# Kernel tuning notes

Hardware: AMD Instinct MI355X
Metric: run time of the kernel (lower is better)

Reference implementation:

```python
import jax, jax.numpy as jnp
import numpy as np

NEG_SLOPE = 0.2
CHUNK = 64  # target-node chunk size to bound the [B,c,N,H,D] intermediate


def layer_norm(x, g, b, eps=1e-5):
    mu = jnp.mean(x, axis=-1, keepdims=True)
    var = jnp.mean((x - mu) ** 2, axis=-1, keepdims=True)
    return (x - mu) / jnp.sqrt(var + eps) * g + b


def gatv2_dense(x, Wl, bl, Wr, br, att, bias):
    """GATv2 (PyG semantics, concat=True) on a fully-connected graph with self-loops.
    x: [B,N,Fin]; att: [H,D]. Returns [B,N,H*D].
    e_ij = att_h . leaky_relu(xl_j + xr_i); softmax over sources j; out_i = sum_j a_ij xl_j.
    """
    B, N, _ = x.shape
    H, D = att.shape
    xl = (x @ Wl + bl).reshape(B, N, H, D)  # source-side (lin_l)
    xr = (x @ Wr + br).reshape(B, N, H, D)  # target-side (lin_r)
    nc = N // CHUNK
    xr_ch = jnp.moveaxis(xr.reshape(B, nc, CHUNK, H, D), 1, 0)  # [nc,B,c,H,D]

    @jax.checkpoint
    def per_chunk(xr_c):  # xr_c: [B,c,H,D]
        z = jax.nn.leaky_relu(xr_c[:, :, None] + xl[:, None], NEG_SLOPE)  # [B,c,N,H,D]
        e = jnp.einsum('bcjhd,hd->bcjh', z, att)
        a = jax.nn.softmax(e, axis=2)  # softmax over sources j
        return jnp.einsum('bcjh,bjhd->bchd', a, xl)

    out = jax.lax.map(per_chunk, xr_ch)  # [nc,B,c,H,D]
    return jnp.moveaxis(out, 0, 1).reshape(B, N, H * D) + bias


def setup_inputs() -> dict:
    key = jax.random.key(0)
    ks = jax.random.split(key, 12)
    B, N, Fin, Hd, H, Do = 4, 2048, 32, 32, 4, 32
    f32 = jnp.float32

    def glorot(k, shape, fan_in):
        return jax.random.normal(k, shape, f32) * (1.0 / np.sqrt(fan_in))

    return {
        'x': jax.random.normal(ks[0], (B, N, Fin), f32),
        'embedding': jax.random.normal(ks[1], (N, Hd), f32),
        # layer 1: in=Fin, heads=H, head dim=Hd
        'Wl1': glorot(ks[2], (Fin, H * Hd), Fin), 'bl1': jnp.zeros((H * Hd,), f32),
        'Wr1': glorot(ks[3], (Fin, H * Hd), Fin), 'br1': jnp.zeros((H * Hd,), f32),
        'att1': glorot(ks[4], (H, Hd), Hd), 'bias1': jnp.zeros((H * Hd,), f32),
        'ln1_g': jnp.ones((H * Hd,), f32), 'ln1_b': jnp.zeros((H * Hd,), f32),
        # layer 2: in=H*Hd, heads=H, head dim=Do
        'Wl2': glorot(ks[5], (H * Hd, H * Do), H * Hd), 'bl2': jnp.zeros((H * Do,), f32),
        'Wr2': glorot(ks[6], (H * Hd, H * Do), H * Hd), 'br2': jnp.zeros((H * Do,), f32),
        'att2': glorot(ks[7], (H, Do), Do), 'bias2': jnp.zeros((H * Do,), f32),
        'ln2_g': jnp.ones((H * Do,), f32), 'ln2_b': jnp.zeros((H * Do,), f32),
    }


def reference(x, embedding, Wl1, bl1, Wr1, br1, att1, bias1, ln1_g, ln1_b,
              Wl2, bl2, Wr2, br2, att2, bias2, ln2_g, ln2_b):
    # AdaptiveAdjacency: cosine-similarity gram matrix. Its values are generically
    # all nonzero, so adj[b].nonzero() yields a fully-connected edge list including
    # self-loops; only the connectivity (dense) is consumed downstream.
    ne = embedding / jnp.linalg.norm(embedding, axis=1, keepdims=True)
    adj = ne @ ne.T  # [N,N]; connectivity only (dense), values unused by GATv2
    del adj

    h = layer_norm(gatv2_dense(x, Wl1, bl1, Wr1, br1, att1, bias1), ln1_g, ln1_b)
    h = jax.nn.relu(h)
    # dropout(p=0.3) is identity in eval mode
    out = layer_norm(gatv2_dense(h, Wl2, bl2, Wr2, br2, att2, bias2), ln2_g, ln2_b)
    return out
```

## Files before the change

### kernel.cpp

```cpp
#include <hip/hip_runtime.h>
#include <math.h>

#define LOG2E 1.4426950408889634f

#if __has_builtin(__builtin_amdgcn_exp2f)
#define EXP2(x) __builtin_amdgcn_exp2f(x)
#else
#define EXP2(x) exp2f(x)
#endif

constexpr int B_ = 4, N_ = 2048, H_ = 4, D_ = 32, HD_ = 128;
constexpr int BH_ = B_ * H_;
constexpr int ROWS_ = BH_ * N_;
constexpr size_t M_ = (size_t)ROWS_ * D_;

typedef float v4f __attribute__((ext_vector_type(4)));
typedef _Float16 h2 __attribute__((ext_vector_type(2)));

static __device__ __forceinline__ h2 habs2(h2 z) {
    unsigned int t = __builtin_bit_cast(unsigned int, z) & 0x7FFF7FFFu;
    return __builtin_bit_cast(h2, t);
}
static __device__ __forceinline__ h2 hadd2u(unsigned int a, unsigned int b) {
    return __builtin_bit_cast(h2, a) + __builtin_bit_cast(h2, b);
}
static __device__ __forceinline__ h2 u2h(unsigned int a) {
    return __builtin_bit_cast(h2, a);
}

__global__ __launch_bounds__(256) void k_linear(
    const float* __restrict__ x,
    const float* __restrict__ Wl, const float* __restrict__ bl,
    const float* __restrict__ Wr, const float* __restrict__ br,
    float* __restrict__ xl, unsigned short* __restrict__ xlh,
    unsigned short* __restrict__ xrh, unsigned int* __restrict__ xlpT, int K)
{
    __shared__ __align__(16) float xs[32 * 128];
    const int tid = threadIdx.x;
    const int r0 = blockIdx.x * 32;
    const float4* src = (const float4*)(x + (size_t)r0 * K);
    float4* dst = (float4*)xs;
    for (int idx = tid; idx < 8 * K; idx += 256) dst[idx] = src[idx];
    __syncthreads();

    const int c  = tid & 127;
    const int rg = tid >> 7;
    float accl[16], accr[16];
    const float blv = bl[c], brv = br[c];
    #pragma unroll
    for (int r = 0; r < 16; r++) { accl[r] = blv; accr[r] = brv; }
    #pragma unroll 8
    for (int k = 0; k < K; k++) {
        const float wl = Wl[k * HD_ + c];
        const float wr = Wr[k * HD_ + c];
        #pragma unroll
        for (int r = 0; r < 16; r++) {
            const float xv = xs[(rg * 16 + r) * K + k];
            accl[r] = fmaf(xv, wl, accl[r]);
            accr[r] = fmaf(xv, wr, accr[r]);
        }
    }
    const int h = c >> 5, d = c & 31;
    #pragma unroll
    for (int r = 0; r < 16; r++) {
        const int row = r0 + rg * 16 + r;
        const int b = row >> 11, n = row & (N_ - 1);
        const size_t o = (((size_t)(b * H_ + h)) * N_ + n) * D_ + d;
        xl[o] = accl[r];
        xlh[o] = __builtin_bit_cast(unsigned short, (_Float16)accl[r]);
        xrh[o] = __builtin_bit_cast(unsigned short, (_Float16)accr[r]);
    }
    #pragma unroll
    for (int r = 0; r < 16; r += 2) {
        const int row = r0 + rg * 16 + r;
        const int b = row >> 11, n = row & (N_ - 1);
        h2 pr;
        pr.x = (_Float16)accl[r];
        pr.y = (_Float16)accl[r + 1];
        const size_t o = (((size_t)(b * H_ + h)) * (N_ / 2) + (n >> 1)) * D_ + d;
        xlpT[o] = __builtin_bit_cast(unsigned int, pr);
    }
}

__global__ __launch_bounds__(256) void k_u(
    const float* __restrict__ xl, const float* __restrict__ att,
    float* __restrict__ u)
{
    const int idx = blockIdx.x * 256 + threadIdx.x;
    const int h = (idx / N_) & (H_ - 1);
    const float4* a4 = (const float4*)(att + h * D_);
    const float4* l4 = (const float4*)(xl + (size_t)idx * D_);
    float su = 0.f;
    #pragma unroll
    for (int q = 0; q < 8; q++) {
        const float4 a = a4[q], lv = l4[q];
        su += a.x * lv.x + a.y * lv.y + a.z * lv.z + a.w * lv.w;
    }
    u[idx] = 0.6f * LOG2E * su;
}

__global__ __launch_bounds__(512) void k_bound(
    const unsigned int* __restrict__ xlh, const unsigned int* __restrict__ xrh,
    const float* __restrict__ u, const float* __restrict__ att,
    float* __restrict__ bound, unsigned int* __restrict__ tch)
{
    __shared__ float redA[16][33];
    __shared__ float redB[16][33];
    __shared__ float clv[32];
    __shared__ float tca[32];
    __shared__ float redu[512];
    const int bh = blockIdx.x, h = bh & (H_ - 1), t = threadIdx.x;

    if (bh < H_ && t < 16) {
        h2 v;
        v.x = (_Float16)(att[bh * D_ + 2 * t]     * (0.4f * LOG2E));
        v.y = (_Float16)(att[bh * D_ + 2 * t + 1] * (0.4f * LOG2E));
        tch[bh * 16 + t] = __builtin_bit_cast(unsigned int, v);
    }
    if (t < 16) {
        _Float16 a = (_Float16)(att[h * D_ + 2 * t]     * (0.4f * LOG2E));
        _Float16 b = (_Float16)(att[h * D_ + 2 * t + 1] * (0.4f * LOG2E));
        tca[2 * t]     = fabsf((float)a);
        tca[2 * t + 1] = fabsf((float)b);
    }
    const unsigned int* xb = xlh + (size_t)bh * N_ * 16;
    const int p = t & 15, rg = t >> 4;
    float m0 = 0.f, m1 = 0.f;
    for (int r = rg; r < N_; r += 32) {
        h2 z = __builtin_bit_cast(h2, xb[r * 16 + p] & 0x7FFF7FFFu);
        m0 = fmaxf(m0, (float)z.x);
        m1 = fmaxf(m1, (float)z.y);
    }
    redA[p][rg] = m0; redB[p][rg] = m1;
    const float* ub = u + (size_t)bh * N_;
    float um = -1e30f;
    for (int r = t; r < N_; r += 512) um = fmaxf(um, ub[r]);
    redu[t] = um;
    __syncthreads();
    if (t < 16) {
        float a = 0.f, b = 0.f;
        for (int g = 0; g < 32; g++) { a = fmaxf(a, redA[t][g]); b = fmaxf(b, redB[t][g]); }
        clv[2 * t] = a; clv[2 * t + 1] = b;
    }
    for (int s = 256; s > 0; s >>= 1) {
        if (t < s) redu[t] = fmaxf(redu[t], redu[t + s]);
        __syncthreads();
    }
    const float umax = redu[0];
    const unsigned int* xrb = xrh + (size_t)bh * N_ * 16;
    for (int r = t; r < N_; r += 512) {
        float s = 0.f;
        #pragma unroll
        for (int k = 0; k < 16; k++) {
            h2 z = __builtin_bit_cast(h2, xrb[r * 16 + k] & 0x7FFF7FFFu);
            s += tca[2 * k] * (clv[2 * k] + (float)z.x)
               + tca[2 * k + 1] * (clv[2 * k + 1] + (float)z.y);
        }
        bound[bh * N_ + r] = umax + s + 0.25f;
    }
}

__global__ __launch_bounds__(256)
__attribute__((amdgpu_waves_per_eu(3, 4)))
void k_attn(
    const unsigned int* __restrict__ xlh,
    const unsigned int* __restrict__ xlpT,
    const unsigned int* __restrict__ xrh,
    const float* __restrict__ u, const float* __restrict__ bound,
    const unsigned int* __restrict__ tch,
    float* __restrict__ P, float* __restrict__ lb, int jlen)
{
    const int tid = threadIdx.x, lane = tid & 63, wid = tid >> 6;
    const int t128 = blockIdx.x & 127, part = blockIdx.x >> 7;
    const int bh = t128 >> 3;
    const int h  = bh & (H_ - 1);
    const int row = bh * N_ + (t128 & 7) * 256 + wid * 64 + lane;

    unsigned int tcs[16];
    #pragma unroll
    for (int k = 0; k < 16; k++)
        tcs[k] = __builtin_amdgcn_readfirstlane(tch[h * 16 + k]);

    unsigned int xrp[16];
    {
        const uint4* s = (const uint4*)(xrh + (size_t)row * 16);
        const uint4 a = s[0], b = s[1], c = s[2], d = s[3];
        xrp[0]=a.x; xrp[1]=a.y; xrp[2]=a.z; xrp[3]=a.w;
        xrp[4]=b.x; xrp[5]=b.y; xrp[6]=b.z; xrp[7]=b.w;
        xrp[8]=c.x; xrp[9]=c.y; xrp[10]=c.z; xrp[11]=c.w;
        xrp[12]=d.x; xrp[13]=d.y; xrp[14]=d.z; xrp[15]=d.w;
    }
    const float negb = -bound[row];

    float l = 0.f;
    float o[32];
    #pragma unroll
    for (int k = 0; k < 32; k++) o[k] = 0.f;

    const unsigned int* xlh_b = xlh + (size_t)bh * N_ * 16;
    const unsigned int* xlt_b = xlpT + (size_t)bh * (N_ / 2) * 32;
    const float* u_b = u + (size_t)bh * N_;

    const int jpb = (part * jlen) >> 1, jpe = jpb + (jlen >> 1);
    for (int jp = jpb; jp < jpe; jp++) {
        const unsigned int* w0 = xlh_b + (size_t)(2 * jp) * 16;
        const unsigned int* w1 = w0 + 16;
        float e0 = u_b[2 * jp]     + negb;
        float f0 = 0.f, e1 = u_b[2 * jp + 1] + negb, f1 = 0.f;
        #pragma unroll
        for (int k = 0; k < 16; k += 2) {
            e0 = __builtin_amdgcn_fdot2(habs2(hadd2u(w0[k],     xrp[k])),     u2h(tcs[k]),     e0, false);
            f0 = __builtin_amdgcn_fdot2(habs2(hadd2u(w0[k + 1], xrp[k + 1])), u2h(tcs[k + 1]), f0, false);
            e1 = __builtin_amdgcn_fdot2(habs2(hadd2u(w1[k],     xrp[k])),     u2h(tcs[k]),     e1, false);
            f1 = __builtin_amdgcn_fdot2(habs2(hadd2u(w1[k + 1], xrp[k + 1])), u2h(tcs[k + 1]), f1, false);
        }
        const float p0 = EXP2(e0 + f0);
        const float p1 = EXP2(e1 + f1);
        const h2 p01 = __builtin_bit_cast(h2, __builtin_amdgcn_cvt_pkrtz(p0, p1));
        h2 ones; ones.x = (_Float16)1.f; ones.y = (_Float16)1.f;
        l = __builtin_amdgcn_fdot2(p01, ones, l, false);
        const unsigned int* vp = xlt_b + (size_t)jp * 32;
        #pragma unroll
        for (int d = 0; d < 32; d++)
            o[d] = __builtin_amdgcn_fdot2(p01, u2h(vp[d]), o[d], false);
    }

    float* Pp = P + (size_t)part * M_ + (size_t)row * D_;
    #pragma unroll
    for (int k = 0; k < 8; k++) {
        v4f w;
        w.x = o[4*k]; w.y = o[4*k+1]; w.z = o[4*k+2]; w.w = o[4*k+3];
        ((v4f*)Pp)[k] = w;
    }
    lb[part * ROWS_ + row] = l;
}

template <int JS>
__global__ __launch_bounds__(64) void k_comb_ln(
    const float* __restrict__ P, const float* __restrict__ lb,
    const float* __restrict__ bias, const float* __restrict__ g,
    const float* __restrict__ bta, float* __restrict__ outp, int do_relu)
{
    const int row = blockIdx.x;
    const int b = row >> 11, n = row & (N_ - 1);
    const int t = threadIdx.x;
    const int c0 = t, c1 = t + 64;
    const int bh0 = b * H_ + (c0 >> 5), bh1 = b * H_ + (c1 >> 5);
    const size_t i0 = ((size_t)bh0 * N_ + n) * D_ + (c0 & 31);
    const size_t i1 = ((size_t)bh1 * N_ + n) * D_ + (c1 & 31);
    float a0 = 0.f, a1 = 0.f, L0 = 0.f, L1 = 0.f;
    #pragma unroll
    for (int s = 0; s < JS; s++) {
        a0 += P[(size_t)s * M_ + i0];
        a1 += P[(size_t)s * M_ + i1];
        L0 += lb[s * ROWS_ + bh0 * N_ + n];
        L1 += lb[s * ROWS_ + bh1 * N_ + n];
    }
    const float x0 = a0 / L0 + bias[c0];
    const float x1 = a1 / L1 + bias[c1];
    float s = x0 + x1;
    #pragma unroll
    for (int w = 1; w < 64; w <<= 1) s += __shfl_xor(s, w);
    const float mu = s * (1.f / 128.f);
    const float d0 = x0 - mu, d1 = x1 - mu;
    float q = d0 * d0 + d1 * d1;
    #pragma unroll
    for (int w = 1; w < 64; w <<= 1) q += __shfl_xor(q, w);
    const float rstd = rsqrtf(q * (1.f / 128.f) + 1e-5f);
    float y0 = d0 * rstd * g[c0] + bta[c0];
    float y1 = d1 * rstd * g[c1] + bta[c1];
    if (do_relu) { y0 = fmaxf(y0, 0.f); y1 = fmaxf(y1, 0.f); }
    outp[(size_t)row * HD_ + c0] = y0;
    outp[(size_t)row * HD_ + c1] = y1;
}

extern "C" void kernel_launch(void* const* d_in, const int* in_sizes, int n_in,
                              void* d_out, int out_size, void* d_ws, size_t ws_size,
                              hipStream_t stream) {
    const float* x    = (const float*)d_in[0];
    const float* Wl1  = (const float*)d_in[2];
    const float* bl1  = (const float*)d_in[3];
    const float* Wr1  = (const float*)d_in[4];
    const float* br1  = (const float*)d_in[5];
    const float* att1 = (const float*)d_in[6];
    const float* bias1= (const float*)d_in[7];
    const float* ln1g = (const float*)d_in[8];
    const float* ln1b = (const float*)d_in[9];
    const float* Wl2  = (const float*)d_in[10];
    const float* bl2  = (const float*)d_in[11];
    const float* Wr2  = (const float*)d_in[12];
    const float* br2  = (const float*)d_in[13];
    const float* att2 = (const float*)d_in[14];
    const float* bias2= (const float*)d_in[15];
    const float* ln2g = (const float*)d_in[16];
    const float* ln2b = (const float*)d_in[17];

    float* ws = (float*)d_ws;
    float* xl = ws;
    unsigned short* xlh = (unsigned short*)(xl + M_);
    unsigned short* xrh = xlh + M_;
    unsigned int* xlpT = (unsigned int*)(xrh + M_);
    float* u     = xl + (size_t)(2.5 * M_);
    float* bound = u + ROWS_;
    unsigned int* tch = (unsigned int*)(bound + ROWS_);

    int js = 1;
    for (int cand = 8; cand >= 1; cand >>= 1) {
        const size_t need = ((size_t)(3.5 * M_) + 2 * ROWS_ + 64
                             + (size_t)cand * (M_ + ROWS_)) * sizeof(float);
        if (ws_size >= need) { js = cand; break; }
    }
    const int jlen = N_ / js;

    float* P  = (float*)(tch + 64);
    float* lb = P + (size_t)js * M_;
    float* h  = lb + (size_t)js * ROWS_;
    float* outf = (float*)d_out;

    const int BN = B_ * N_;
    k_linear<<<BN / 32, 256, 0, stream>>>(x, Wl1, bl1, Wr1, br1, xl, xlh, xrh, xlpT, 32);
    k_u<<<ROWS_ / 256, 256, 0, stream>>>(xl, att1, u);
    k_bound<<<BH_, 512, 0, stream>>>((const unsigned int*)xlh, (const unsigned int*)xrh,
                                     u, att1, bound, tch);
    k_attn<<<128 * js, 256, 0, stream>>>((const unsigned int*)xlh, xlpT,
                                         (const unsigned int*)xrh, u, bound, tch, P, lb, jlen);
    if      (js == 8) k_comb_ln<8><<<BN, 64, 0, stream>>>(P, lb, bias1, ln1g, ln1b, h, 1);
    else if (js == 4) k_comb_ln<4><<<BN, 64, 0, stream>>>(P, lb, bias1, ln1g, ln1b, h, 1);
    else if (js == 2) k_comb_ln<2><<<BN, 64, 0, stream>>>(P, lb, bias1, ln1g, ln1b, h, 1);
    else              k_comb_ln<1><<<BN, 64, 0, stream>>>(P, lb, bias1, ln1g, ln1b, h, 1);
    k_linear<<<BN / 32, 256, 0, stream>>>(h, Wl2, bl2, Wr2, br2, xl, xlh, xrh, xlpT, 128);
    k_u<<<ROWS_ / 256, 256, 0, stream>>>(xl, att2, u);
    k_bound<<<BH_, 512, 0, stream>>>((const unsigned int*)xlh, (const unsigned int*)xrh,
                                     u, att2, bound, tch);
    k_attn<<<128 * js, 256, 0, stream>>>((const unsigned int*)xlh, xlpT,
                                         (const unsigned int*)xrh, u, bound, tch, P, lb, jlen);
    if      (js == 8) k_comb_ln<8><<<BN, 64, 0, stream>>>(P, lb, bias2, ln2g, ln2b, outf, 0);
    else if (js == 4) k_comb_ln<4><<<BN, 64, 0, stream>>>(P, lb, bias2, ln2g, ln2b, outf, 0);
    else if (js == 2) k_comb_ln<2><<<BN, 64, 0, stream>>>(P, lb, bias2, ln2g, ln2b, outf, 0);
    else              k_comb_ln<1><<<BN, 64, 0, stream>>>(P, lb, bias2, ln2g, ln2b, outf, 0);
}
```

Baseline: 489.3 us.

## Software-pipeline attention loop with double-buffered loads and SGPR-operand dot asm

```diff
diff --git a/kernel.cpp b/kernel.cpp
--- a/kernel.cpp
+++ b/kernel.cpp
@@ -17,16 +17,12 @@
 typedef float v4f __attribute__((ext_vector_type(4)));
 typedef _Float16 h2 __attribute__((ext_vector_type(2)));
 
-static __device__ __forceinline__ h2 habs2(h2 z) {
-    unsigned int t = __builtin_bit_cast(unsigned int, z) & 0x7FFF7FFFu;
-    return __builtin_bit_cast(h2, t);
-}
-static __device__ __forceinline__ h2 hadd2u(unsigned int a, unsigned int b) {
-    return __builtin_bit_cast(h2, a) + __builtin_bit_cast(h2, b);
-}
-static __device__ __forceinline__ h2 u2h(unsigned int a) {
-    return __builtin_bit_cast(h2, a);
-}
+static __device__ __forceinline__ unsigned int absadd2(unsigned int a, unsigned int b) {
+    h2 s = __builtin_bit_cast(h2, a) + __builtin_bit_cast(h2, b);
+    return __builtin_bit_cast(unsigned int, s) & 0x7FFF7FFFu;
+}
+#define SDOT(acc, a, sb) asm("v_dot2_f32_f16 %0, %1, %2, %0" : "+v"(acc) : "v"(a), "s"(sb))
+#define VDOT(acc, a, vb) asm("v_dot2_f32_f16 %0, %1, %2, %0" : "+v"(acc) : "v"(a), "v"(vb))
 
 __global__ __launch_bounds__(256) void k_linear(
     const float* __restrict__ x,
@@ -161,7 +157,7 @@
 }
 
 __global__ __launch_bounds__(256)
-__attribute__((amdgpu_waves_per_eu(3, 4)))
+__attribute__((amdgpu_waves_per_eu(2, 4)))
 void k_attn(
     const unsigned int* __restrict__ xlh,
     const unsigned int* __restrict__ xlpT,
@@ -190,7 +186,8 @@
         xrp[8]=c.x; xrp[9]=c.y; xrp[10]=c.z; xrp[11]=c.w;
         xrp[12]=d.x; xrp[13]=d.y; xrp[14]=d.z; xrp[15]=d.w;
     }
-    const float negb = -bound[row];
+    const float negb = 12.0f - bound[row];
+    const unsigned int ONES2 = 0x3C003C00u;
 
     float l = 0.f;
     float o[32];
@@ -202,28 +199,86 @@
     const float* u_b = u + (size_t)bh * N_;
 
     const int jpb = (part * jlen) >> 1, jpe = jpb + (jlen >> 1);
-    for (int jp = jpb; jp < jpe; jp++) {
-        const unsigned int* w0 = xlh_b + (size_t)(2 * jp) * 16;
-        const unsigned int* w1 = w0 + 16;
-        float e0 = u_b[2 * jp]     + negb;
-        float f0 = 0.f, e1 = u_b[2 * jp + 1] + negb, f1 = 0.f;
-        #pragma unroll
-        for (int k = 0; k < 16; k += 2) {
-            e0 = __builtin_amdgcn_fdot2(habs2(hadd2u(w0[k],     xrp[k])),     u2h(tcs[k]),     e0, false);
-            f0 = __builtin_amdgcn_fdot2(habs2(hadd2u(w0[k + 1], xrp[k + 1])), u2h(tcs[k + 1]), f0, false);
-            e1 = __builtin_amdgcn_fdot2(habs2(hadd2u(w1[k],     xrp[k])),     u2h(tcs[k]),     e1, false);
-            f1 = __builtin_amdgcn_fdot2(habs2(hadd2u(w1[k + 1], xrp[k + 1])), u2h(tcs[k + 1]), f1, false);
-        }
-        const float p0 = EXP2(e0 + f0);
-        const float p1 = EXP2(e1 + f1);
-        const h2 p01 = __builtin_bit_cast(h2, __builtin_amdgcn_cvt_pkrtz(p0, p1));
-        h2 ones; ones.x = (_Float16)1.f; ones.y = (_Float16)1.f;
-        l = __builtin_amdgcn_fdot2(p01, ones, l, false);
-        const unsigned int* vp = xlt_b + (size_t)jp * 32;
-        #pragma unroll
-        for (int d = 0; d < 32; d++)
-            o[d] = __builtin_amdgcn_fdot2(p01, u2h(vp[d]), o[d], false);
-    }
+
+#define LOADS(S0, S1, S2, S3, S4, S5, S6, S7, UU0, UU1, JP)                    \
+    {                                                                           \
+        const uint4* _w = (const uint4*)(xlh_b + (size_t)(2 * (JP)) * 16);     \
+        S0 = _w[0]; S1 = _w[1]; S2 = _w[2]; S3 = _w[3];                        \
+        S4 = _w[4]; S5 = _w[5]; S6 = _w[6]; S7 = _w[7];                        \
+        UU0 = u_b[2 * (JP)]; UU1 = u_b[2 * (JP) + 1];                          \
+    }
+#define COMPUTE(S0, S1, S2, S3, S4, S5, S6, S7, UU0, UU1, JP)                  \
+    {                                                                           \
+        const uint4* _vp = (const uint4*)(xlt_b + (size_t)(JP) * 32);          \
+        uint4 _v0 = _vp[0], _v1 = _vp[1], _v2 = _vp[2], _v3 = _vp[3];          \
+        float _e0 = UU0 + negb, _f0 = 0.f, _e1 = UU1 + negb, _f1 = 0.f;        \
+        SDOT(_e0, absadd2(S0.x, xrp[0]),  tcs[0]);                             \
+        SDOT(_f0, absadd2(S0.y, xrp[1]),  tcs[1]);                             \
+        SDOT(_e0, absadd2(S0.z, xrp[2]),  tcs[2]);                             \
+        SDOT(_f0, absadd2(S0.w, xrp[3]),  tcs[3]);                             \
+        SDOT(_e0, absadd2(S1.x, xrp[4]),  tcs[4]);                             \
+        SDOT(_f0, absadd2(S1.y, xrp[5]),  tcs[5]);                             \
+        SDOT(_e0, absadd2(S1.z, xrp[6]),  tcs[6]);                             \
+        SDOT(_f0, absadd2(S1.w, xrp[7]),  tcs[7]);                             \
+        SDOT(_e0, absadd2(S2.x, xrp[8]),  tcs[8]);                             \
+        SDOT(_f0, absadd2(S2.y, xrp[9]),  tcs[9]);                             \
+        SDOT(_e0, absadd2(S2.z, xrp[10]), tcs[10]);                            \
+        SDOT(_f0, absadd2(S2.w, xrp[11]), tcs[11]);                            \
+        SDOT(_e0, absadd2(S3.x, xrp[12]), tcs[12]);                            \
+        SDOT(_f0, absadd2(S3.y, xrp[13]), tcs[13]);                            \
+        SDOT(_e0, absadd2(S3.z, xrp[14]), tcs[14]);                            \
+        SDOT(_f0, absadd2(S3.w, xrp[15]), tcs[15]);                            \
+        SDOT(_e1, absadd2(S4.x, xrp[0]),  tcs[0]);                             \
+        SDOT(_f1, absadd2(S4.y, xrp[1]),  tcs[1]);                             \
+        SDOT(_e1, absadd2(S4.z, xrp[2]),  tcs[2]);                             \
+        SDOT(_f1, absadd2(S4.w, xrp[3]),  tcs[3]);                             \
+        SDOT(_e1, absadd2(S5.x, xrp[4]),  tcs[4]);                             \
+        SDOT(_f1, absadd2(S5.y, xrp[5]),  tcs[5]);                             \
+        SDOT(_e1, absadd2(S5.z, xrp[6]),  tcs[6]);                             \
+        SDOT(_f1, absadd2(S5.w, xrp[7]),  tcs[7]);                             \
+        SDOT(_e1, absadd2(S6.x, xrp[8]),  tcs[8]);                             \
+        SDOT(_f1, absadd2(S6.y, xrp[9]),  tcs[9]);                             \
+        SDOT(_e1, absadd2(S6.z, xrp[10]), tcs[10]);                            \
+        SDOT(_f1, absadd2(S6.w, xrp[11]), tcs[11]);                            \
+        SDOT(_e1, absadd2(S7.x, xrp[12]), tcs[12]);                            \
+        SDOT(_f1, absadd2(S7.y, xrp[13]), tcs[13]);                            \
+        SDOT(_e1, absadd2(S7.z, xrp[14]), tcs[14]);                            \
+        SDOT(_f1, absadd2(S7.w, xrp[15]), tcs[15]);                            \
+        const float _p0 = EXP2(_e0 + _f0);                                     \
+        const float _p1 = EXP2(_e1 + _f1);                                     \
+        const unsigned int _p01 = __builtin_bit_cast(unsigned int,             \
+            __builtin_amdgcn_cvt_pkrtz(_p0, _p1));                             \
+        VDOT(l, _p01, ONES2);                                                  \
+        VDOT(o[0],  _p01, _v0.x); VDOT(o[1],  _p01, _v0.y);                    \
+        VDOT(o[2],  _p01, _v0.z); VDOT(o[3],  _p01, _v0.w);                    \
+        VDOT(o[4],  _p01, _v1.x); VDOT(o[5],  _p01, _v1.y);                    \
+        VDOT(o[6],  _p01, _v1.z); VDOT(o[7],  _p01, _v1.w);                    \
+        VDOT(o[8],  _p01, _v2.x); VDOT(o[9],  _p01, _v2.y);                    \
+        VDOT(o[10], _p01, _v2.z); VDOT(o[11], _p01, _v2.w);                    \
+        VDOT(o[12], _p01, _v3.x); VDOT(o[13], _p01, _v3.y);                    \
+        VDOT(o[14], _p01, _v3.z); VDOT(o[15], _p01, _v3.w);                    \
+        uint4 _v4 = _vp[4], _v5 = _vp[5], _v6 = _vp[6], _v7 = _vp[7];          \
+        VDOT(o[16], _p01, _v4.x); VDOT(o[17], _p01, _v4.y);                    \
+        VDOT(o[18], _p01, _v4.z); VDOT(o[19], _p01, _v4.w);                    \
+        VDOT(o[20], _p01, _v5.x); VDOT(o[21], _p01, _v5.y);                    \
+        VDOT(o[22], _p01, _v5.z); VDOT(o[23], _p01, _v5.w);                    \
+        VDOT(o[24], _p01, _v6.x); VDOT(o[25], _p01, _v6.y);                    \
+        VDOT(o[26], _p01, _v6.z); VDOT(o[27], _p01, _v6.w);                    \
+        VDOT(o[28], _p01, _v7.x); VDOT(o[29], _p01, _v7.y);                    \
+        VDOT(o[30], _p01, _v7.z); VDOT(o[31], _p01, _v7.w);                    \
+    }
+
+    uint4 A0, A1, A2, A3, A4, A5, A6, A7; float AU0, AU1;
+    uint4 B0, B1, B2, B3, B4, B5, B6, B7; float BU0, BU1;
+    LOADS(A0, A1, A2, A3, A4, A5, A6, A7, AU0, AU1, jpb);
+    for (int jp = jpb; jp < jpe; jp += 2) {
+        LOADS(B0, B1, B2, B3, B4, B5, B6, B7, BU0, BU1, jp + 1);
+        COMPUTE(A0, A1, A2, A3, A4, A5, A6, A7, AU0, AU1, jp);
+        LOADS(A0, A1, A2, A3, A4, A5, A6, A7, AU0, AU1, jp + 2);
+        COMPUTE(B0, B1, B2, B3, B4, B5, B6, B7, BU0, BU1, jp + 1);
+    }
+#undef LOADS
+#undef COMPUTE
 
     float* Pp = P + (size_t)part * M_ + (size_t)row * D_;
     #pragma unroll
```

Result: no change. 492.0 us (+0.6%).

## Stage source tiles in LDS and use inline-asm dot2 with SGPR operands in attention

Applied to the files above, without the earlier changes.

```diff
diff --git a/kernel.cpp b/kernel.cpp
--- a/kernel.cpp
+++ b/kernel.cpp
@@ -17,16 +17,12 @@
 typedef float v4f __attribute__((ext_vector_type(4)));
 typedef _Float16 h2 __attribute__((ext_vector_type(2)));
 
-static __device__ __forceinline__ h2 habs2(h2 z) {
-    unsigned int t = __builtin_bit_cast(unsigned int, z) & 0x7FFF7FFFu;
-    return __builtin_bit_cast(h2, t);
-}
-static __device__ __forceinline__ h2 hadd2u(unsigned int a, unsigned int b) {
-    return __builtin_bit_cast(h2, a) + __builtin_bit_cast(h2, b);
-}
-static __device__ __forceinline__ h2 u2h(unsigned int a) {
-    return __builtin_bit_cast(h2, a);
-}
+static __device__ __forceinline__ unsigned int absadd2(unsigned int a, unsigned int b) {
+    h2 s = __builtin_bit_cast(h2, a) + __builtin_bit_cast(h2, b);
+    return __builtin_bit_cast(unsigned int, s) & 0x7FFF7FFFu;
+}
+#define SDOT(acc, a, sb) asm("v_dot2_f32_f16 %0, %1, %2, %0" : "+v"(acc) : "v"(a), "s"(sb))
+#define VDOT(acc, a, vb) asm("v_dot2_f32_f16 %0, %1, %2, %0" : "+v"(acc) : "v"(a), "v"(vb))
 
 __global__ __launch_bounds__(256) void k_linear(
     const float* __restrict__ x,
@@ -160,9 +156,7 @@
     }
 }
 
-__global__ __launch_bounds__(256)
-__attribute__((amdgpu_waves_per_eu(3, 4)))
-void k_attn(
+__global__ __launch_bounds__(256) void k_attn(
     const unsigned int* __restrict__ xlh,
     const unsigned int* __restrict__ xlpT,
     const unsigned int* __restrict__ xrh,
@@ -170,11 +164,14 @@
     const unsigned int* __restrict__ tch,
     float* __restrict__ P, float* __restrict__ lb, int jlen)
 {
-    const int tid = threadIdx.x, lane = tid & 63, wid = tid >> 6;
+    __shared__ __align__(16) uint4 s_xlh[1024];
+    __shared__ __align__(16) uint4 s_xlt[1024];
+    __shared__ float s_u[256];
+    const int tid = threadIdx.x;
     const int t128 = blockIdx.x & 127, part = blockIdx.x >> 7;
     const int bh = t128 >> 3;
     const int h  = bh & (H_ - 1);
-    const int row = bh * N_ + (t128 & 7) * 256 + wid * 64 + lane;
+    const int row = bh * N_ + (t128 & 7) * 256 + tid;
 
     unsigned int tcs[16];
     #pragma unroll
@@ -190,39 +187,96 @@
         xrp[8]=c.x; xrp[9]=c.y; xrp[10]=c.z; xrp[11]=c.w;
         xrp[12]=d.x; xrp[13]=d.y; xrp[14]=d.z; xrp[15]=d.w;
     }
-    const float negb = -bound[row];
+    const float negb = 12.0f - bound[row];
+    const unsigned int ONES2 = 0x3C003C00u;
 
     float l = 0.f;
     float o[32];
     #pragma unroll
     for (int k = 0; k < 32; k++) o[k] = 0.f;
 
-    const unsigned int* xlh_b = xlh + (size_t)bh * N_ * 16;
-    const unsigned int* xlt_b = xlpT + (size_t)bh * (N_ / 2) * 32;
+    const uint4* gx = (const uint4*)(xlh + (size_t)bh * N_ * 16);
+    const uint4* gv = (const uint4*)(xlpT + (size_t)bh * (N_ / 2) * 32);
     const float* u_b = u + (size_t)bh * N_;
 
-    const int jpb = (part * jlen) >> 1, jpe = jpb + (jlen >> 1);
-    for (int jp = jpb; jp < jpe; jp++) {
-        const unsigned int* w0 = xlh_b + (size_t)(2 * jp) * 16;
-        const unsigned int* w1 = w0 + 16;
-        float e0 = u_b[2 * jp]     + negb;
-        float f0 = 0.f, e1 = u_b[2 * jp + 1] + negb, f1 = 0.f;
+    const int jbeg = part * jlen;
+    for (int jt = 0; jt < jlen; jt += 256) {
+        if (jt) __syncthreads();
+        const int j0 = jbeg + jt;
         #pragma unroll
-        for (int k = 0; k < 16; k += 2) {
-            e0 = __builtin_amdgcn_fdot2(habs2(hadd2u(w0[k],     xrp[k])),     u2h(tcs[k]),     e0, false);
-            f0 = __builtin_amdgcn_fdot2(habs2(hadd2u(w0[k + 1], xrp[k + 1])), u2h(tcs[k + 1]), f0, false);
-            e1 = __builtin_amdgcn_fdot2(habs2(hadd2u(w1[k],     xrp[k])),     u2h(tcs[k]),     e1, false);
-            f1 = __builtin_amdgcn_fdot2(habs2(hadd2u(w1[k + 1], xrp[k + 1])), u2h(tcs[k + 1]), f1, false);
+        for (int k = 0; k < 4; k++)
+            s_xlh[tid + 256 * k] = gx[(size_t)j0 * 4 + tid + 256 * k];
+        #pragma unroll
+        for (int k = 0; k < 4; k++)
+            s_xlt[tid + 256 * k] = gv[(size_t)(j0 >> 1) * 8 + tid + 256 * k];
+        s_u[tid] = u_b[j0 + tid];
+        __syncthreads();
+
+        for (int ljp = 0; ljp < 128; ljp++) {
+            const uint4 S0 = s_xlh[8 * ljp + 0], S1 = s_xlh[8 * ljp + 1];
+            const uint4 S2 = s_xlh[8 * ljp + 2], S3 = s_xlh[8 * ljp + 3];
+            const uint4 S4 = s_xlh[8 * ljp + 4], S5 = s_xlh[8 * ljp + 5];
+            const uint4 S6 = s_xlh[8 * ljp + 6], S7 = s_xlh[8 * ljp + 7];
+            float e0 = s_u[2 * ljp] + negb, f0 = 0.f;
+            float e1 = s_u[2 * ljp + 1] + negb, f1 = 0.f;
+            SDOT(e0, absadd2(S0.x, xrp[0]),  tcs[0]);
+            SDOT(f0, absadd2(S0.y, xrp[1]),  tcs[1]);
+            SDOT(e0, absadd2(S0.z, xrp[2]),  tcs[2]);
+            SDOT(f0, absadd2(S0.w, xrp[3]),  tcs[3]);
+            SDOT(e0, absadd2(S1.x, xrp[4]),  tcs[4]);
+            SDOT(f0, absadd2(S1.y, xrp[5]),  tcs[5]);
+            SDOT(e0, absadd2(S1.z, xrp[6]),  tcs[6]);
+            SDOT(f0, absadd2(S1.w, xrp[7]),  tcs[7]);
+            SDOT(e0, absadd2(S2.x, xrp[8]),  tcs[8]);
+            SDOT(f0, absadd2(S2.y, xrp[9]),  tcs[9]);
+            SDOT(e0, absadd2(S2.z, xrp[10]), tcs[10]);
+            SDOT(f0, absadd2(S2.w, xrp[11]), tcs[11]);
+            SDOT(e0, absadd2(S3.x, xrp[12]), tcs[12]);
+            SDOT(f0, absadd2(S3.y, xrp[13]), tcs[13]);
+            SDOT(e0, absadd2(S3.z, xrp[14]), tcs[14]);
+            SDOT(f0, absadd2(S3.w, xrp[15]), tcs[15]);
+            SDOT(e1, absadd2(S4.x, xrp[0]),  tcs[0]);
+            SDOT(f1, absadd2(S4.y, xrp[1]),  tcs[1]);
+            SDOT(e1, absadd2(S4.z, xrp[2]),  tcs[2]);
+            SDOT(f1, absadd2(S4.w, xrp[3]),  tcs[3]);
+            SDOT(e1, absadd2(S5.x, xrp[4]),  tcs[4]);
+            SDOT(f1, absadd2(S5.y, xrp[5]),  tcs[5]);
+            SDOT(e1, absadd2(S5.z, xrp[6]),  tcs[6]);
+            SDOT(f1, absadd2(S5.w, xrp[7]),  tcs[7]);
+            SDOT(e1, absadd2(S6.x, xrp[8]),  tcs[8]);
+            SDOT(f1, absadd2(S6.y, xrp[9]),  tcs[9]);
+            SDOT(e1, absadd2(S6.z, xrp[10]), tcs[10]);
+            SDOT(f1, absadd2(S6.w, xrp[11]), tcs[11]);
+            SDOT(e1, absadd2(S7.x, xrp[12]), tcs[12]);
+            SDOT(f1, absadd2(S7.y, xrp[13]), tcs[13]);
+            SDOT(e1, absadd2(S7.z, xrp[14]), tcs[14]);
+            SDOT(f1, absadd2(S7.w, xrp[15]), tcs[15]);
+            const float p0 = EXP2(e0 + f0);
+            const float p1 = EXP2(e1 + f1);
+            const unsigned int p01 = __builtin_bit_cast(unsigned int,
+                __builtin_amdgcn_cvt_pkrtz(p0, p1));
+            VDOT(l, p01, ONES2);
+            const uint4 V0 = s_xlt[8 * ljp + 0], V1 = s_xlt[8 * ljp + 1];
+            const uint4 V2 = s_xlt[8 * ljp + 2], V3 = s_xlt[8 * ljp + 3];
+            VDOT(o[0],  p01, V0.x); VDOT(o[1],  p01, V0.y);
+            VDOT(o[2],  p01, V0.z); VDOT(o[3],  p01, V0.w);
+            VDOT(o[4],  p01, V1.x); VDOT(o[5],  p01, V1.y);
+            VDOT(o[6],  p01, V1.z); VDOT(o[7],  p01, V1.w);
+            VDOT(o[8],  p01, V2.x); VDOT(o[9],  p01, V2.y);
+            VDOT(o[10], p01, V2.z); VDOT(o[11], p01, V2.w);
+            VDOT(o[12], p01, V3.x); VDOT(o[13], p01, V3.y);
+            VDOT(o[14], p01, V3.z); VDOT(o[15], p01, V3.w);
+            const uint4 V4 = s_xlt[8 * ljp + 4], V5 = s_xlt[8 * ljp + 5];
+            const uint4 V6 = s_xlt[8 * ljp + 6], V7 = s_xlt[8 * ljp + 7];
+            VDOT(o[16], p01, V4.x); VDOT(o[17], p01, V4.y);
+            VDOT(o[18], p01, V4.z); VDOT(o[19], p01, V4.w);
+            VDOT(o[20], p01, V5.x); VDOT(o[21], p01, V5.y);
+            VDOT(o[22], p01, V5.z); VDOT(o[23], p01, V5.w);
+            VDOT(o[24], p01, V6.x); VDOT(o[25], p01, V6.y);
+            VDOT(o[26], p01, V6.z); VDOT(o[27], p01, V6.w);
+            VDOT(o[28], p01, V7.x); VDOT(o[29], p01, V7.y);
+            VDOT(o[30], p01, V7.z); VDOT(o[31], p01, V7.w);
         }
-        const float p0 = EXP2(e0 + f0);
-        const float p1 = EXP2(e1 + f1);
-        const h2 p01 = __builtin_bit_cast(h2, __builtin_amdgcn_cvt_pkrtz(p0, p1));
-        h2 ones; ones.x = (_Float16)1.f; ones.y = (_Float16)1.f;
-        l = __builtin_amdgcn_fdot2(p01, ones, l, false);
-        const unsigned int* vp = xlt_b + (size_t)jp * 32;
-        #pragma unroll
-        for (int d = 0; d < 32; d++)
-            o[d] = __builtin_amdgcn_fdot2(p01, u2h(vp[d]), o[d], false);
     }
 
     float* Pp = P + (size_t)part * M_ + (size_t)row * D_;
```

Measured after the change: 429.7 us. 12.2% less time.

## Stage source rows in LDS and use inline-asm fma_mix for attention

Applied to the files above, without the earlier changes.

```diff
diff --git a/kernel.cpp b/kernel.cpp
--- a/kernel.cpp
+++ b/kernel.cpp
@@ -17,23 +17,12 @@
 typedef float v4f __attribute__((ext_vector_type(4)));
 typedef _Float16 h2 __attribute__((ext_vector_type(2)));
 
-static __device__ __forceinline__ h2 habs2(h2 z) {
-    unsigned int t = __builtin_bit_cast(unsigned int, z) & 0x7FFF7FFFu;
-    return __builtin_bit_cast(h2, t);
-}
-static __device__ __forceinline__ h2 hadd2u(unsigned int a, unsigned int b) {
-    return __builtin_bit_cast(h2, a) + __builtin_bit_cast(h2, b);
-}
-static __device__ __forceinline__ h2 u2h(unsigned int a) {
-    return __builtin_bit_cast(h2, a);
-}
-
 __global__ __launch_bounds__(256) void k_linear(
     const float* __restrict__ x,
     const float* __restrict__ Wl, const float* __restrict__ bl,
     const float* __restrict__ Wr, const float* __restrict__ br,
     float* __restrict__ xl, unsigned short* __restrict__ xlh,
-    unsigned short* __restrict__ xrh, unsigned int* __restrict__ xlpT, int K)
+    unsigned short* __restrict__ xrh, int K)
 {
     __shared__ __align__(16) float xs[32 * 128];
     const int tid = threadIdx.x;
@@ -70,16 +59,6 @@
         xlh[o] = __builtin_bit_cast(unsigned short, (_Float16)accl[r]);
         xrh[o] = __builtin_bit_cast(unsigned short, (_Float16)accr[r]);
     }
-    #pragma unroll
-    for (int r = 0; r < 16; r += 2) {
-        const int row = r0 + rg * 16 + r;
-        const int b = row >> 11, n = row & (N_ - 1);
-        h2 pr;
-        pr.x = (_Float16)accl[r];
-        pr.y = (_Float16)accl[r + 1];
-        const size_t o = (((size_t)(b * H_ + h)) * (N_ / 2) + (n >> 1)) * D_ + d;
-        xlpT[o] = __builtin_bit_cast(unsigned int, pr);
-    }
 }
 
 __global__ __launch_bounds__(256) void k_u(
@@ -160,26 +139,41 @@
     }
 }
 
-__global__ __launch_bounds__(256)
-__attribute__((amdgpu_waves_per_eu(3, 4)))
-void k_attn(
+
+#define SG(K, EA, EB)                                                          \
+    "v_pk_add_f16 %[z], %[s" K "], %[x" K "]\n\t"                              \
+    "v_and_b32 %[z], %[mk], %[z]\n\t"                                          \
+    "v_fma_mix_f32 %[" EA "], %[tl" K "], %[z], %[" EA "] op_sel:[0,0,0] op_sel_hi:[0,1,0]\n\t" \
+    "v_fma_mix_f32 %[" EB "], %[th" K "], %[z], %[" EB "] op_sel:[0,1,0] op_sel_hi:[0,1,0]\n\t"
+
+#define PVG(KL, KH, SK)                                                        \
+    "v_fma_mix_f32 %[o" KL "], %[p], %[s" SK "], %[o" KL "] op_sel:[0,0,0] op_sel_hi:[0,1,0]\n\t" \
+    "v_fma_mix_f32 %[o" KH "], %[p], %[s" SK "], %[o" KH "] op_sel:[0,1,0] op_sel_hi:[0,1,0]\n\t"
+
+__global__ __launch_bounds__(256) void k_attn(
     const unsigned int* __restrict__ xlh,
-    const unsigned int* __restrict__ xlpT,
     const unsigned int* __restrict__ xrh,
     const float* __restrict__ u, const float* __restrict__ bound,
     const unsigned int* __restrict__ tch,
     float* __restrict__ P, float* __restrict__ lb, int jlen)
 {
-    const int tid = threadIdx.x, lane = tid & 63, wid = tid >> 6;
+    __shared__ __align__(16) uint4 s_xlh[1024];
+    __shared__ float s_u[256];
+    __shared__ float s_pad[4096];
+    const int tid = threadIdx.x;
     const int t128 = blockIdx.x & 127, part = blockIdx.x >> 7;
     const int bh = t128 >> 3;
     const int h  = bh & (H_ - 1);
-    const int row = bh * N_ + (t128 & 7) * 256 + wid * 64 + lane;
-
-    unsigned int tcs[16];
-    #pragma unroll
-    for (int k = 0; k < 16; k++)
-        tcs[k] = __builtin_amdgcn_readfirstlane(tch[h * 16 + k]);
+    const int row = bh * N_ + (t128 & 7) * 256 + tid;
+    if (jlen < 0) s_pad[tid] = 0.f;
+
+    float tf[32];
+    #pragma unroll
+    for (int k = 0; k < 16; k++) {
+        const h2 t2 = __builtin_bit_cast(h2, tch[h * 16 + k]);
+        tf[2 * k]     = (float)t2.x;
+        tf[2 * k + 1] = (float)t2.y;
+    }
 
     unsigned int xrp[16];
     {
@@ -191,38 +185,82 @@
         xrp[12]=d.x; xrp[13]=d.y; xrp[14]=d.z; xrp[15]=d.w;
     }
     const float negb = -bound[row];
+    const unsigned int kAbsMask = 0x7FFF7FFFu;
 
     float l = 0.f;
     float o[32];
     #pragma unroll
     for (int k = 0; k < 32; k++) o[k] = 0.f;
 
-    const unsigned int* xlh_b = xlh + (size_t)bh * N_ * 16;
-    const unsigned int* xlt_b = xlpT + (size_t)bh * (N_ / 2) * 32;
+    const uint4* gx = (const uint4*)(xlh + (size_t)bh * N_ * 16);
     const float* u_b = u + (size_t)bh * N_;
 
-    const int jpb = (part * jlen) >> 1, jpe = jpb + (jlen >> 1);
-    for (int jp = jpb; jp < jpe; jp++) {
-        const unsigned int* w0 = xlh_b + (size_t)(2 * jp) * 16;
-        const unsigned int* w1 = w0 + 16;
-        float e0 = u_b[2 * jp]     + negb;
-        float f0 = 0.f, e1 = u_b[2 * jp + 1] + negb, f1 = 0.f;
+    const int jbeg = part * jlen;
+    for (int jt = 0; jt < jlen; jt += 256) {
+        if (jt) __syncthreads();
+        const int j0 = jbeg + jt;
         #pragma unroll
-        for (int k = 0; k < 16; k += 2) {
-            e0 = __builtin_amdgcn_fdot2(habs2(hadd2u(w0[k],     xrp[k])),     u2h(tcs[k]),     e0, false);
-            f0 = __builtin_amdgcn_fdot2(habs2(hadd2u(w0[k + 1], xrp[k + 1])), u2h(tcs[k + 1]), f0, false);
-            e1 = __builtin_amdgcn_fdot2(habs2(hadd2u(w1[k],     xrp[k])),     u2h(tcs[k]),     e1, false);
-            f1 = __builtin_amdgcn_fdot2(habs2(hadd2u(w1[k + 1], xrp[k + 1])), u2h(tcs[k + 1]), f1, false);
+        for (int k = 0; k < 4; k++)
+            s_xlh[tid + 256 * k] = gx[(size_t)j0 * 4 + tid + 256 * k];
+        s_u[tid] = u_b[j0 + tid];
+        __syncthreads();
+
+        for (int j = 0; j < 256; j++) {
+            const uint4 S0 = s_xlh[4 * j + 0], S1 = s_xlh[4 * j + 1];
+            const uint4 S2 = s_xlh[4 * j + 2], S3 = s_xlh[4 * j + 3];
+            float e0 = s_u[j] + negb, e1 = 0.f, e2 = 0.f, e3 = 0.f;
+            unsigned int zz;
+            asm(SG("0",  "e0", "e1") SG("1",  "e2", "e3")
+                SG("2",  "e0", "e1") SG("3",  "e2", "e3")
+                SG("4",  "e0", "e1") SG("5",  "e2", "e3")
+                SG("6",  "e0", "e1") SG("7",  "e2", "e3")
+                SG("8",  "e0", "e1") SG("9",  "e2", "e3")
+                SG("10", "e0", "e1") SG("11", "e2", "e3")
+                SG("12", "e0", "e1") SG("13", "e2", "e3")
+                SG("14", "e0", "e1") SG("15", "e2", "e3")
+                : [e0]"+v"(e0), [e1]"+v"(e1), [e2]"+v"(e2), [e3]"+v"(e3),
+                  [z]"=&v"(zz)
+                : [s0]"v"(S0.x),  [s1]"v"(S0.y),  [s2]"v"(S0.z),  [s3]"v"(S0.w),
+                  [s4]"v"(S1.x),  [s5]"v"(S1.y),  [s6]"v"(S1.z),  [s7]"v"(S1.w),
+                  [s8]"v"(S2.x),  [s9]"v"(S2.y),  [s10]"v"(S2.z), [s11]"v"(S2.w),
+                  [s12]"v"(S3.x), [s13]"v"(S3.y), [s14]"v"(S3.z), [s15]"v"(S3.w),
+                  [x0]"v"(xrp[0]),   [x1]"v"(xrp[1]),   [x2]"v"(xrp[2]),   [x3]"v"(xrp[3]),
+                  [x4]"v"(xrp[4]),   [x5]"v"(xrp[5]),   [x6]"v"(xrp[6]),   [x7]"v"(xrp[7]),
+                  [x8]"v"(xrp[8]),   [x9]"v"(xrp[9]),   [x10]"v"(xrp[10]), [x11]"v"(xrp[11]),
+                  [x12]"v"(xrp[12]), [x13]"v"(xrp[13]), [x14]"v"(xrp[14]), [x15]"v"(xrp[15]),
+                  [tl0]"v"(tf[0]),   [th0]"v"(tf[1]),   [tl1]"v"(tf[2]),   [th1]"v"(tf[3]),
+                  [tl2]"v"(tf[4]),   [th2]"v"(tf[5]),   [tl3]"v"(tf[6]),   [th3]"v"(tf[7]),
+                  [tl4]"v"(tf[8]),   [th4]"v"(tf[9]),   [tl5]"v"(tf[10]),  [th5]"v"(tf[11]),
+                  [tl6]"v"(tf[12]),  [th6]"v"(tf[13]),  [tl7]"v"(tf[14]),  [th7]"v"(tf[15]),
+                  [tl8]"v"(tf[16]),  [th8]"v"(tf[17]),  [tl9]"v"(tf[18]),  [th9]"v"(tf[19]),
+                  [tl10]"v"(tf[20]), [th10]"v"(tf[21]), [tl11]"v"(tf[22]), [th11]"v"(tf[23]),
+                  [tl12]"v"(tf[24]), [th12]"v"(tf[25]), [tl13]"v"(tf[26]), [th13]"v"(tf[27]),
+                  [tl14]"v"(tf[28]), [th14]"v"(tf[29]), [tl15]"v"(tf[30]), [th15]"v"(tf[31]),
+                  [mk]"s"(kAbsMask));
+            const float p = EXP2((e0 + e1) + (e2 + e3));
+            l += p;
+            asm(PVG("0",  "1",  "0")  PVG("2",  "3",  "1")
+                PVG("4",  "5",  "2")  PVG("6",  "7",  "3")
+                PVG("8",  "9",  "4")  PVG("10", "11", "5")
+                PVG("12", "13", "6")  PVG("14", "15", "7")
+                PVG("16", "17", "8")  PVG("18", "19", "9")
+                PVG("20", "21", "10") PVG("22", "23", "11")
+                PVG("24", "25", "12") PVG("26", "27", "13")
+                PVG("28", "29", "14") PVG("30", "31", "15")
+                : [o0]"+v"(o[0]),   [o1]"+v"(o[1]),   [o2]"+v"(o[2]),   [o3]"+v"(o[3]),
+                  [o4]"+v"(o[4]),   [o5]"+v"(o[5]),   [o6]"+v"(o[6]),   [o7]"+v"(o[7]),
+                  [o8]"+v"(o[8]),   [o9]"+v"(o[9]),   [o10]"+v"(o[10]), [o11]"+v"(o[11]),
+                  [o12]"+v"(o[12]), [o13]"+v"(o[13]), [o14]"+v"(o[14]), [o15]"+v"(o[15]),
+                  [o16]"+v"(o[16]), [o17]"+v"(o[17]), [o18]"+v"(o[18]), [o19]"+v"(o[19]),
+                  [o20]"+v"(o[20]), [o21]"+v"(o[21]), [o22]"+v"(o[22]), [o23]"+v"(o[23]),
+                  [o24]"+v"(o[24]), [o25]"+v"(o[25]), [o26]"+v"(o[26]), [o27]"+v"(o[27]),
+                  [o28]"+v"(o[28]), [o29]"+v"(o[29]), [o30]"+v"(o[30]), [o31]"+v"(o[31])
+                : [p]"v"(p),
+                  [s0]"v"(S0.x),  [s1]"v"(S0.y),  [s2]"v"(S0.z),  [s3]"v"(S0.w),
+                  [s4]"v"(S1.x),  [s5]"v"(S1.y),  [s6]"v"(S1.z),  [s7]"v"(S1.w),
+                  [s8]"v"(S2.x),  [s9]"v"(S2.y),  [s10]"v"(S2.z), [s11]"v"(S2.w),
+                  [s12]"v"(S3.x), [s13]"v"(S3.y), [s14]"v"(S3.z), [s15]"v"(S3.w));
         }
-        const float p0 = EXP2(e0 + f0);
-        const float p1 = EXP2(e1 + f1);
-        const h2 p01 = __builtin_bit_cast(h2, __builtin_amdgcn_cvt_pkrtz(p0, p1));
-        h2 ones; ones.x = (_Float16)1.f; ones.y = (_Float16)1.f;
-        l = __builtin_amdgcn_fdot2(p01, ones, l, false);
-        const unsigned int* vp = xlt_b + (size_t)jp * 32;
-        #pragma unroll
-        for (int d = 0; d < 32; d++)
-            o[d] = __builtin_amdgcn_fdot2(p01, u2h(vp[d]), o[d], false);
     }
 
     float* Pp = P + (size_t)part * M_ + (size_t)row * D_;
@@ -299,14 +337,13 @@
     float* xl = ws;
     unsigned short* xlh = (unsigned short*)(xl + M_);
     unsigned short* xrh = xlh + M_;
-    unsigned int* xlpT = (unsigned int*)(xrh + M_);
-    float* u     = xl + (size_t)(2.5 * M_);
+    float* u     = xl + 2 * M_;
     float* bound = u + ROWS_;
     unsigned int* tch = (unsigned int*)(bound + ROWS_);
 
     int js = 1;
     for (int cand = 8; cand >= 1; cand >>= 1) {
-        const size_t need = ((size_t)(3.5 * M_) + 2 * ROWS_ + 64
+        const size_t need = ((size_t)3 * M_ + 2 * ROWS_ + 64
                              + (size_t)cand * (M_ + ROWS_)) * sizeof(float);
         if (ws_size >= need) { js = cand; break; }
     }
@@ -318,21 +355,21 @@
     float* outf = (float*)d_out;
 
     const int BN = B_ * N_;
-    k_linear<<<BN / 32, 256, 0, stream>>>(x, Wl1, bl1, Wr1, br1, xl, xlh, xrh, xlpT, 32);
+    k_linear<<<BN / 32, 256, 0, stream>>>(x, Wl1, bl1, Wr1, br1, xl, xlh, xrh, 32);
     k_u<<<ROWS_ / 256, 256, 0, stream>>>(xl, att1, u);
     k_bound<<<BH_, 512, 0, stream>>>((const unsigned int*)xlh, (const unsigned int*)xrh,
                                      u, att1, bound, tch);
-    k_attn<<<128 * js, 256, 0, stream>>>((const unsigned int*)xlh, xlpT,
+    k_attn<<<128 * js, 256, 0, stream>>>((const unsigned int*)xlh,
                                          (const unsigned int*)xrh, u, bound, tch, P, lb, jlen);
     if      (js == 8) k_comb_ln<8><<<BN, 64, 0, stream>>>(P, lb, bias1, ln1g, ln1b, h, 1);
     else if (js == 4) k_comb_ln<4><<<BN, 64, 0, stream>>>(P, lb, bias1, ln1g, ln1b, h, 1);
     else if (js == 2) k_comb_ln<2><<<BN, 64, 0, stream>>>(P, lb, bias1, ln1g, ln1b, h, 1);
     else              k_comb_ln<1><<<BN, 64, 0, stream>>>(P, lb, bias1, ln1g, ln1b, h, 1);
-    k_linear<<<BN / 32, 256, 0, stream>>>(h, Wl2, bl2, Wr2, br2, xl, xlh, xrh, xlpT, 128);
+    k_linear<<<BN / 32, 256, 0, stream>>>(h, Wl2, bl2, Wr2, br2, xl, xlh, xrh, 128);
     k_u<<<ROWS_ / 256, 256, 0, stream>>>(xl, att2, u);
     k_bound<<<BH_, 512, 0, stream>>>((const unsigned int*)xlh, (const unsigned int*)xrh,
                                      u, att2, bound, tch);
-    k_attn<<<128 * js, 256, 0, stream>>>((const unsigned int*)xlh, xlpT,
+    k_attn<<<128 * js, 256, 0, stream>>>((const unsigned int*)xlh,
                                          (const unsigned int*)xrh, u, bound, tch, P, lb, jlen);
     if      (js == 8) k_comb_ln<8><<<BN, 64, 0, stream>>>(P, lb, bias2, ln2g, ln2b, outf, 0);
     else if (js == 4) k_comb_ln<4><<<BN, 64, 0, stream>>>(P, lb, bias2, ln2g, ln2b, outf, 0);
```

Measured after the change: 546.7 us. +11.7%, slower.
